# Performance work log

Measured on AMD Instinct MI355X. Metric: run time of the kernel, lower is better.

Reference implementation:

```python
import jax, jax.numpy as jnp
import numpy as np

EPS = 1e-5
NEG_SLOPE = 0.2


def knn(x, k):
    # x: (B, C, N). pairwise_distance = -||xi - xj||^2, topk -> nearest neighbors.
    xt = jnp.swapaxes(x, 1, 2)                       # (B, N, C)
    inner = -2.0 * jnp.matmul(xt, x)                 # (B, N, N)
    xx = jnp.sum(x * x, axis=1, keepdims=True)       # (B, 1, N)
    pd = -xx - inner - jnp.swapaxes(xx, 1, 2)        # (B, N, N)
    return jax.lax.top_k(pd, k)[1]                   # (B, N, k) int32


def get_graph_feature(x, k):
    # x: (B, C, N) -> (B, N, k, 2C) edge features [neighbor - center, center]
    idx = knn(x, k)
    xt = jnp.swapaxes(x, 1, 2)                       # (B, N, C)
    nb = jax.vmap(lambda f, i: f[i])(xt, idx)        # (B, N, k, C) gather
    center = xt[:, :, None, :]                       # (B, N, 1, C)
    return jnp.concatenate(
        [nb - center, jnp.broadcast_to(center, nb.shape)], axis=-1)


def edge_conv(x, w, k):
    # conv_2d with kernel 1: 1x1 conv (no bias) + InstanceNorm2d + LeakyReLU, then max over k
    feat = get_graph_feature(x, k)                   # (B, N, k, 2C)
    y = jnp.einsum('bnkc,oc->bonk', feat, w)         # (B, O, N, k)
    mean = jnp.mean(y, axis=(2, 3), keepdims=True)
    var = jnp.var(y, axis=(2, 3), keepdims=True)
    y = (y - mean) * jax.lax.rsqrt(var + EPS)        # InstanceNorm2d (no affine)
    y = jnp.where(y >= 0, y, NEG_SLOPE * y)
    return jnp.max(y, axis=-1)                       # (B, O, N)


def setup_inputs() -> dict:
    key = jax.random.key(0)
    ks = jax.random.split(key, 8)
    B, N = 16, 2048
    s = 0.05
    return {
        'x': jax.random.normal(ks[0], (B, 3, N), dtype=jnp.float32),
        'w1': jax.random.normal(ks[1], (64, 6), dtype=jnp.float32) * s,
        'w2': jax.random.normal(ks[2], (64, 128), dtype=jnp.float32) * s,
        'w3': jax.random.normal(ks[3], (128, 128), dtype=jnp.float32) * s,
        'w4': jax.random.normal(ks[4], (256, 256), dtype=jnp.float32) * s,
        'w5': jax.random.normal(ks[5], (512, 512), dtype=jnp.float32) * s,
        'bn5_gamma': jnp.ones((512,), dtype=jnp.float32),
        'bn5_beta': jnp.zeros((512,), dtype=jnp.float32),
    }


def reference(x, w1, w2, w3, w4, w5, bn5_gamma, bn5_beta):
    k = 20
    x1 = edge_conv(x, w1, k)                         # (B, 64, N)
    x2 = edge_conv(x1, w2, k)                        # (B, 64, N)
    x3 = edge_conv(x2, w3, k)                        # (B, 128, N)
    x4 = edge_conv(x3, w4, k)                        # (B, 256, N)
    x_cat = jnp.concatenate([x1, x2, x3, x4], axis=1)  # (B, 512, N)
    y = jnp.einsum('bcn,oc->bon', x_cat, w5)         # conv5, (B, 512, N)
    # BatchNorm1d (training-mode batch stats) over (B, N)
    mean = jnp.mean(y, axis=(0, 2), keepdims=True)
    var = jnp.var(y, axis=(0, 2), keepdims=True)
    y = (y - mean) * jax.lax.rsqrt(var + EPS)
    y = y * bn5_gamma[None, :, None] + bn5_beta[None, :, None]
    y = jnp.where(y >= 0, y, NEG_SLOPE * y)
    feat = jnp.concatenate([jnp.max(y, axis=2), jnp.mean(y, axis=2)], axis=1)  # (B, 1024)
    return feat
```

## Files before the change

### kernel.cpp

```cpp
#include <hip/hip_runtime.h>

#define NN 2048
#define NB 16
#define KK 20
#define EPSF 1e-5f

typedef unsigned long long ull;
typedef _Float16 v8h __attribute__((ext_vector_type(8)));
typedef float v4f __attribute__((ext_vector_type(4)));

__device__ __forceinline__ float shflx_f(float v, int m) { return __shfl_xor(v, m, 64); }
__device__ __forceinline__ ull shflx_u64(ull v, int m) {
  int lo = __shfl_xor((int)(unsigned)v, m, 64);
  int hi = __shfl_xor((int)(unsigned)(v >> 32), m, 64);
  return (((ull)(unsigned)hi) << 32) | (unsigned)lo;
}
__device__ __forceinline__ ull packkey(float s, int n) {
  unsigned u = __float_as_uint(s);
  u = (u & 0x80000000u) ? ~u : (u | 0x80000000u);
  return (((ull)u) << 32) | (unsigned)(2047 - n);
}

__global__ __launch_bounds__(256) void prep_kernel(const float* __restrict__ x,
    _Float16* __restrict__ xh, _Float16* __restrict__ xl, float* __restrict__ xx,
    int C, int KB, long bstride)
{
  const int b = blockIdx.y;
  const int n = blockIdx.x * 256 + threadIdx.x;
  const float* xb = x + (size_t)b * bstride;
  const int Cp = KB * 32;
  _Float16* ph = xh + ((size_t)b * NN + n) * Cp;
  _Float16* pl = xl + ((size_t)b * NN + n) * Cp;
  float s = 0.f;
  for (int kb = 0; kb < KB; kb++) {
    for (int g = 0; g < 4; g++) {
      v8h hv, lv;
#pragma unroll
      for (int j = 0; j < 8; j++) {
        int c = kb * 32 + g * 8 + j;
        float v = (c < C) ? xb[(size_t)c * NN + n] : 0.f;
        _Float16 h = (_Float16)v;
        hv[j] = h;
        lv[j] = (_Float16)(v - (float)h);
        s = fmaf(v, v, s);
      }
      *(v8h*)(ph + kb * 32 + g * 8) = hv;
      *(v8h*)(pl + kb * 32 + g * 8) = lv;
    }
  }
  xx[b * NN + n] = s;
}

template<int KB>
__device__ __forceinline__ void tile_scores(const v8h (&Bh)[KB], const v8h (&Bl)[KB],
    const v8h (&Ah)[4][KB], const v8h (&Al)[4][KB], float xv, v4f (&out)[4])
{
#pragma unroll
  for (int a = 0; a < 4; a++) {
    v4f a0 = {0.f, 0.f, 0.f, 0.f};
    v4f a1 = {0.f, 0.f, 0.f, 0.f};
#pragma unroll
    for (int kb = 0; kb < KB; kb++) {
      v4f& acc = (kb & 1) ? a1 : a0;
      acc = __builtin_amdgcn_mfma_f32_16x16x32_f16(Ah[a][kb], Bh[kb], acc, 0, 0, 0);
      acc = __builtin_amdgcn_mfma_f32_16x16x32_f16(Ah[a][kb], Bl[kb], acc, 0, 0, 0);
      acc = __builtin_amdgcn_mfma_f32_16x16x32_f16(Al[a][kb], Bh[kb], acc, 0, 0, 0);
    }
    v4f s = a0 + a1;
#pragma unroll
    for (int j = 0; j < 4; j++) out[a][j] = s[j] - 0.5f * xv;
  }
}

template<int KB>
__global__ __launch_bounds__(256, 1) void knn2(
    const _Float16* __restrict__ xh, const _Float16* __restrict__ xl,
    const float* __restrict__ xxg, ull* __restrict__ slistG, int* __restrict__ cntG)
{
  __shared__ float gmL[256][33];
  __shared__ float tauL[256];
  __shared__ int scnt[256];

  const int t = threadIdx.x;
  const int lane = t & 63;
  const int wave = t >> 6;
  const int col = lane & 15;
  const int quad = lane >> 4;
  const int quad8 = quad * 8;
  const int b = blockIdx.x >> 1;
  const int chunk = blockIdx.x & 1;
  const int qg = blockIdx.y;
  const int Cp = KB * 32;
  const int cb = chunk * 1024;
  const _Float16* xhb = xh + (size_t)b * NN * Cp;
  const _Float16* xlb = xl + (size_t)b * NN * Cp;
  const float* xxb = xxg + b * NN;

  v8h Ah[4][KB], Al[4][KB];
  const int qw = qg * 256 + wave * 64;
#pragma unroll
  for (int a = 0; a < 4; a++) {
    const _Float16* pa = xhb + (size_t)(qw + a * 16 + col) * Cp + quad8;
    const _Float16* pb = xlb + (size_t)(qw + a * 16 + col) * Cp + quad8;
#pragma unroll
    for (int kb = 0; kb < KB; kb++) {
      Ah[a][kb] = *(const v8h*)(pa + kb * 32);
      Al[a][kb] = *(const v8h*)(pb + kb * 32);
    }
  }

  v8h Bh[2][KB], Bl[2][KB];
  float xvb[2];
  auto loadB = [&](int slot, int tt) {
    int t2 = tt < 63 ? tt : 63;
    int n = cb + t2 * 16 + col;
    const _Float16* pb = xhb + (size_t)n * Cp + quad8;
    const _Float16* pl = xlb + (size_t)n * Cp + quad8;
#pragma unroll
    for (int kb = 0; kb < KB; kb++) {
      Bh[slot][kb] = *(const v8h*)(pb + kb * 32);
      Bl[slot][kb] = *(const v8h*)(pl + kb * 32);
    }
    xvb[slot] = xxb[n];
  };

  float gm[4][8];
#pragma unroll
  for (int a = 0; a < 4; a++)
#pragma unroll
    for (int j = 0; j < 8; j++) gm[a][j] = -3.4e38f;

  loadB(0, 0);
  for (int tt = 0; tt < 64; tt += 2) {
    loadB(1, tt + 1);
    {
      v4f out[4];
      tile_scores<KB>(Bh[0], Bl[0], Ah, Al, xvb[0], out);
#pragma unroll
      for (int a = 0; a < 4; a++)
#pragma unroll
        for (int j = 0; j < 4; j++) gm[a][j * 2] = fmaxf(gm[a][j * 2], out[a][j]);
    }
    loadB(0, tt + 2);
    {
      v4f out[4];
      tile_scores<KB>(Bh[1], Bl[1], Ah, Al, xvb[1], out);
#pragma unroll
      for (int a = 0; a < 4; a++)
#pragma unroll
        for (int j = 0; j < 4; j++) gm[a][j * 2 + 1] = fmaxf(gm[a][j * 2 + 1], out[a][j]);
    }
  }

#pragma unroll
  for (int a = 0; a < 4; a++)
#pragma unroll
    for (int j = 0; j < 4; j++) {
      int qi = wave * 64 + a * 16 + quad * 4 + j;
      gmL[qi][col * 2 + 0] = gm[a][j * 2 + 0];
      gmL[qi][col * 2 + 1] = gm[a][j * 2 + 1];
    }
  scnt[t] = 0;
  asm volatile("s_waitcnt lgkmcnt(0)" ::: "memory");

  for (int r = 0; r < 32; r++) {
    const int q = wave * 64 + r * 2 + (lane >> 5);
    const int idx = lane & 31;
    float v = gmL[q][idx];
#pragma unroll
    for (int kk = 2; kk <= 32; kk <<= 1) {
#pragma unroll
      for (int m = kk >> 1; m >= 1; m >>= 1) {
        float o = shflx_f(v, m);
        bool keepmax = ((idx & kk) == 0) == ((idx & m) == 0);
        v = keepmax ? fmaxf(v, o) : fminf(v, o);
      }
    }
    if (idx == 19) tauL[q] = v;
  }
  asm volatile("s_waitcnt lgkmcnt(0)" ::: "memory");

  float tq[4][4];
#pragma unroll
  for (int a = 0; a < 4; a++)
#pragma unroll
    for (int j = 0; j < 4; j++) tq[a][j] = tauL[wave * 64 + a * 16 + quad * 4 + j];

  ull* slB = slistG + (((size_t)b * NN + qg * 256) * 2 + chunk) * 64;
  loadB(0, 0);
  for (int tt = 0; tt < 64; tt += 2) {
    loadB(1, tt + 1);
    for (int s = 0; s < 2; s++) {
      v4f out[4];
      tile_scores<KB>(s ? Bh[1] : Bh[0], s ? Bl[1] : Bl[0], Ah, Al, xvb[s], out);
      int n = cb + (tt + s) * 16 + col;
#pragma unroll
      for (int a = 0; a < 4; a++)
#pragma unroll
        for (int j = 0; j < 4; j++) {
          float sc = out[a][j];
          if (sc >= tq[a][j]) {
            int qi = wave * 64 + a * 16 + quad * 4 + j;
            int pos = atomicAdd(&scnt[qi], 1);
            if (pos < 64) slB[(size_t)qi * 128 + pos] = packkey(sc, n);
          }
        }
      if (s == 0) loadB(0, tt + 2);
    }
  }
  asm volatile("s_waitcnt lgkmcnt(0)" ::: "memory");
  cntG[((size_t)b * NN + qg * 256 + t) * 2 + chunk] = scnt[t];
}

__global__ __launch_bounds__(256) void knn_merge(const ull* __restrict__ slistG,
    const int* __restrict__ cntG, const _Float16* __restrict__ xh,
    const _Float16* __restrict__ xl, const float* __restrict__ xxg,
    int* __restrict__ idxout, int Cp, int C)
{
  const int lane = threadIdx.x & 63, wave = threadIdx.x >> 6;
  const int b = blockIdx.y;
  const int q = blockIdx.x * 4 + wave;
  const int c0 = cntG[((size_t)b * NN + q) * 2 + 0];
  const int c1 = cntG[((size_t)b * NN + q) * 2 + 1];
  int* op = idxout + ((size_t)b * NN + q) * KK;

  if (c0 <= 64 && c1 <= 64) {
    const ull* s0 = slistG + ((size_t)b * NN + q) * 128;
    const int total = c0 + c1;
    ull e0 = 0, e1 = 0;
    int p0 = lane, p1 = lane + 64;
    if (p0 < total) e0 = (p0 < c0) ? s0[p0] : s0[64 + p0 - c0];
    if (p1 < total) e1 = (p1 < c0) ? s0[p1] : s0[64 + p1 - c0];
    for (int s = 0; s < KK; s++) {
      ull m = e0 > e1 ? e0 : e1;
      ull g = m;
#pragma unroll
      for (int d = 1; d < 64; d <<= 1) { ull o = shflx_u64(g, d); g = o > g ? o : g; }
      if (lane == 0) op[s] = 2047 - (int)(g & 0xFFFFFFFFu);
      if (e0 == g) e0 = 0; else if (e1 == g) e1 = 0;
    }
  } else {
    const _Float16* qh = xh + ((size_t)b * NN + q) * Cp;
    const _Float16* ql = xl + ((size_t)b * NN + q) * Cp;
    const float* xxb = xxg + b * NN;
    float sc[32];
#pragma unroll
    for (int i = 0; i < 32; i++) sc[i] = -0.5f * xxb[lane + 64 * i];
    for (int c = 0; c < C; c++) {
      float qv = (float)qh[c] + (float)ql[c];
      for (int i = 0; i < 32; i++) {
        int n = lane + 64 * i;
        float bv = (float)xh[((size_t)b * NN + n) * Cp + c] + (float)xl[((size_t)b * NN + n) * Cp + c];
        sc[i] = fmaf(qv, bv, sc[i]);
      }
    }
    for (int s = 0; s < KK; s++) {
      ull m = 0; int mi = -1;
      for (int i = 0; i < 32; i++) {
        ull k = packkey(sc[i], lane + 64 * i);
        if (k > m) { m = k; mi = i; }
      }
      ull g = m;
#pragma unroll
      for (int d = 1; d < 64; d <<= 1) { ull o = shflx_u64(g, d); g = o > g ? o : g; }
      if (lane == 0) op[s] = 2047 - (int)(g & 0xFFFFFFFFu);
      if (m == g && mi >= 0) sc[mi] = -3.4e38f;
    }
  }
}

__global__ __launch_bounds__(256) void wcvt_uv(const float* __restrict__ w,
    _Float16* __restrict__ wuh, _Float16* __restrict__ wul,
    _Float16* __restrict__ wvh, _Float16* __restrict__ wvl, int C, int Cp, int O)
{
  int idx = blockIdx.x * 256 + threadIdx.x;
  if (idx >= O * Cp) return;
  int o = idx / Cp, c = idx - o * Cp;
  float a = 0.f, bv = 0.f;
  if (c < C) { a = w[o * 2 * C + c]; bv = w[o * 2 * C + C + c]; }
  float v = bv - a;
  _Float16 ah = (_Float16)a; wuh[idx] = ah; wul[idx] = (_Float16)(a - (float)ah);
  _Float16 vh = (_Float16)v; wvh[idx] = vh; wvl[idx] = (_Float16)(v - (float)vh);
}

__global__ __launch_bounds__(256) void w5cvt(const float* __restrict__ w5,
    _Float16* __restrict__ w5h, _Float16* __restrict__ w5l)
{
  int idx = blockIdx.x * 256 + threadIdx.x;
  float v = w5[idx];
  _Float16 h = (_Float16)v;
  w5h[idx] = h;
  w5l[idx] = (_Float16)(v - (float)h);
}

__global__ __launch_bounds__(256) void y5cvt_kernel(const float* __restrict__ xcat,
    _Float16* __restrict__ xh, _Float16* __restrict__ xl)
{
  const int b = blockIdx.y;
  const int n = blockIdx.x * 256 + threadIdx.x;
  for (int kc = blockIdx.z * 4; kc < blockIdx.z * 4 + 4; kc++) {
    v8h h[4], l[4];
#pragma unroll
    for (int g = 0; g < 4; g++)
#pragma unroll
      for (int j = 0; j < 8; j++) {
        float v = xcat[((size_t)b * 512 + kc * 32 + g * 8 + j) * NN + n];
        _Float16 hh = (_Float16)v;
        h[g][j] = hh;
        l[g][j] = (_Float16)(v - (float)hh);
      }
    size_t base = (((size_t)b * 16 + kc) * NN + n) * 32;
#pragma unroll
    for (int g = 0; g < 4; g++) {
      *(v8h*)(xh + base + g * 8) = h[g];
      *(v8h*)(xl + base + g * 8) = l[g];
    }
  }
}

__global__ __launch_bounds__(256) void y5_mfma(const _Float16* __restrict__ w5h,
    const _Float16* __restrict__ w5l, const _Float16* __restrict__ xh,
    const _Float16* __restrict__ xl, float* __restrict__ y5)
{
  const int lane = threadIdx.x & 63, wave = threadIdx.x >> 6;
  const int col = lane & 15, quad = lane >> 4, quad8 = quad * 8;
  const int b = blockIdx.z;
  const int o0 = blockIdx.x * 256 + wave * 64;
  const int nb0 = blockIdx.y * 128;
  v4f acc[4][8];
#pragma unroll
  for (int a = 0; a < 4; a++)
#pragma unroll
    for (int t = 0; t < 8; t++) acc[a][t] = {0.f, 0.f, 0.f, 0.f};

  for (int kc = 0; kc < 16; kc++) {
    v8h Ah[4], Al[4];
#pragma unroll
    for (int a = 0; a < 4; a++) {
      size_t off = (size_t)(o0 + a * 16 + col) * 512 + kc * 32 + quad8;
      Ah[a] = *(const v8h*)(w5h + off);
      Al[a] = *(const v8h*)(w5l + off);
    }
#pragma unroll
    for (int t = 0; t < 8; t++) {
      int n = nb0 + t * 16 + col;
      size_t boff = (((size_t)b * 16 + kc) * NN + n) * 32 + quad8;
      v8h Bh = *(const v8h*)(xh + boff);
      v8h Bl = *(const v8h*)(xl + boff);
#pragma unroll
      for (int a = 0; a < 4; a++) {
        acc[a][t] = __builtin_amdgcn_mfma_f32_16x16x32_f16(Ah[a], Bh, acc[a][t], 0, 0, 0);
        acc[a][t] = __builtin_amdgcn_mfma_f32_16x16x32_f16(Ah[a], Bl, acc[a][t], 0, 0, 0);
        acc[a][t] = __builtin_amdgcn_mfma_f32_16x16x32_f16(Al[a], Bh, acc[a][t], 0, 0, 0);
      }
    }
  }
#pragma unroll
  for (int a = 0; a < 4; a++)
#pragma unroll
    for (int t = 0; t < 8; t++)
#pragma unroll
      for (int j = 0; j < 4; j++)
        y5[((size_t)b * 512 + o0 + a * 16 + quad * 4 + j) * NN + nb0 + t * 16 + col] = acc[a][t][j];
}

__global__ __launch_bounds__(256) void uv_mfma(const _Float16* __restrict__ wuh,
    const _Float16* __restrict__ wul, const _Float16* __restrict__ wvh,
    const _Float16* __restrict__ wvl, const _Float16* __restrict__ xh,
    const _Float16* __restrict__ xl, float* __restrict__ Uc, float* __restrict__ Vc,
    int Cp, int Och)
{
  const int lane = threadIdx.x & 63, wave = threadIdx.x >> 6;
  const int col = lane & 15, quad = lane >> 4, quad8 = quad * 8;
  const int b = blockIdx.z;
  const int o0 = blockIdx.x * 32;
  const int nb0 = blockIdx.y * 256 + wave * 64;
  v4f aU[2][4], aV[2][4];
#pragma unroll
  for (int a = 0; a < 2; a++)
#pragma unroll
    for (int t = 0; t < 4; t++) { aU[a][t] = {0.f,0.f,0.f,0.f}; aV[a][t] = {0.f,0.f,0.f,0.f}; }

  const int KBr = Cp >> 5;
  for (int kb = 0; kb < KBr; kb++) {
    v8h Uh[2], Ul[2], Vh[2], Vl[2];
#pragma unroll
    for (int a = 0; a < 2; a++) {
      size_t off = (size_t)(o0 + a * 16 + col) * Cp + kb * 32 + quad8;
      Uh[a] = *(const v8h*)(wuh + off);
      Ul[a] = *(const v8h*)(wul + off);
      Vh[a] = *(const v8h*)(wvh + off);
      Vl[a] = *(const v8h*)(wvl + off);
    }
#pragma unroll
    for (int t = 0; t < 4; t++) {
      int n = nb0 + t * 16 + col;
      size_t boff = ((size_t)b * NN + n) * Cp + kb * 32 + quad8;
      v8h Bh = *(const v8h*)(xh + boff);
      v8h Bl = *(const v8h*)(xl + boff);
#pragma unroll
      for (int a = 0; a < 2; a++) {
        aU[a][t] = __builtin_amdgcn_mfma_f32_16x16x32_f16(Uh[a], Bh, aU[a][t], 0, 0, 0);
        aU[a][t] = __builtin_amdgcn_mfma_f32_16x16x32_f16(Uh[a], Bl, aU[a][t], 0, 0, 0);
        aU[a][t] = __builtin_amdgcn_mfma_f32_16x16x32_f16(Ul[a], Bh, aU[a][t], 0, 0, 0);
        aV[a][t] = __builtin_amdgcn_mfma_f32_16x16x32_f16(Vh[a], Bh, aV[a][t], 0, 0, 0);
        aV[a][t] = __builtin_amdgcn_mfma_f32_16x16x32_f16(Vh[a], Bl, aV[a][t], 0, 0, 0);
        aV[a][t] = __builtin_amdgcn_mfma_f32_16x16x32_f16(Vl[a], Bh, aV[a][t], 0, 0, 0);
      }
    }
  }
#pragma unroll
  for (int a = 0; a < 2; a++)
#pragma unroll
    for (int t = 0; t < 4; t++)
#pragma unroll
      for (int j = 0; j < 4; j++) {
        size_t base = ((size_t)b * Och + o0 + a * 16 + quad * 4 + j) * NN + nb0 + t * 16 + col;
        Uc[base] = aU[a][t][j];
        Vc[base] = aV[a][t][j];
      }
}

__global__ __launch_bounds__(256) void edge5(const float* __restrict__ Uc,
    const float* __restrict__ Vc, const int* __restrict__ idx,
    float* __restrict__ xo, int Och)
{
  __shared__ float Ur[2 * 2052];
  __shared__ float red[4][4];
  __shared__ float smv[4];
  const int b = blockIdx.y, o0 = blockIdx.x * 2;
  const int t = threadIdx.x, lane = t & 63, wave = t >> 6;
  for (int r = 0; r < 2; r++)
    for (int i = t; i < NN; i += 256)
      Ur[r * 2052 + i] = Uc[((size_t)b * Och + o0 + r) * NN + i];
  __syncthreads();
  const float* Vp = Vc + ((size_t)b * Och + o0) * NN;
  const int* ib = idx + (size_t)b * NN * KK;
  float s0 = 0, s1 = 0, c0 = 0, c1 = 0;
  for (int n = t; n < NN; n += 256) {
    float v0 = Vp[n], v1 = Vp[NN + n];
    const int* ip = ib + (size_t)n * KK;
#pragma unroll
    for (int j = 0; j < KK; j++) {
      int m = ip[j];
      float y0 = Ur[m] + v0, y1 = Ur[2052 + m] + v1;
      s0 += y0; c0 = fmaf(y0, y0, c0);
      s1 += y1; c1 = fmaf(y1, y1, c1);
    }
  }
  float st[4] = { s0, s1, c0, c1 };
#pragma unroll
  for (int k = 0; k < 4; k++) {
    float a = st[k];
#pragma unroll
    for (int d = 1; d < 64; d <<= 1) a += shflx_f(a, d);
    if (lane == 0) red[k][wave] = a;
  }
  __syncthreads();
  if (t < 2) {
    float a = red[t][0] + red[t][1] + red[t][2] + red[t][3];
    float c = red[2 + t][0] + red[2 + t][1] + red[2 + t][2] + red[2 + t][3];
    const float inv = 1.f / (float)(NN * KK);
    float mu = a * inv;
    float var = fmaxf(c * inv - mu * mu, 0.f);
    smv[t] = mu;
    smv[2 + t] = rsqrtf(var + EPSF);
  }
  __syncthreads();
  const float mu0 = smv[0], mu1 = smv[1], i0 = smv[2], i1 = smv[3];
  for (int n = t; n < NN; n += 256) {
    float v0 = Vp[n], v1 = Vp[NN + n];
    const int* ip = ib + (size_t)n * KK;
    float m0 = -3.4e38f, m1 = m0;
#pragma unroll
    for (int j = 0; j < KK; j++) {
      int m = ip[j];
      m0 = fmaxf(m0, Ur[m] + v0);
      m1 = fmaxf(m1, Ur[2052 + m] + v1);
    }
    float z;
    z = (m0 - mu0) * i0; xo[((size_t)b * 512 + o0 + 0) * NN + n] = z >= 0.f ? z : 0.2f * z;
    z = (m1 - mu1) * i1; xo[((size_t)b * 512 + o0 + 1) * NN + n] = z >= 0.f ? z : 0.2f * z;
  }
}

__global__ __launch_bounds__(256) void bn5stat_kernel(const float* __restrict__ y5,
    float* __restrict__ bn5) {
  __shared__ float rs[4], rq[4];
  const int o = blockIdx.x, t = threadIdx.x, lane = t & 63, wave = t >> 6;
  float s = 0.f, q = 0.f;
  for (int b = 0; b < NB; b++) {
    const float* p = y5 + ((size_t)b * 512 + o) * NN;
    for (int n = t; n < NN; n += 256) { float v = p[n]; s += v; q = fmaf(v, v, q); }
  }
#pragma unroll
  for (int d = 1; d < 64; d <<= 1) { s += shflx_f(s, d); q += shflx_f(q, d); }
  if (lane == 0) { rs[wave] = s; rq[wave] = q; }
  __syncthreads();
  if (t == 0) {
    float S = rs[0] + rs[1] + rs[2] + rs[3];
    float Q = rq[0] + rq[1] + rq[2] + rq[3];
    const float inv = 1.f / (float)(NB * NN);
    float mu = S * inv;
    float var = fmaxf(Q * inv - mu * mu, 0.f);
    bn5[o] = mu;
    bn5[512 + o] = rsqrtf(var + EPSF);
  }
}

__global__ __launch_bounds__(256) void final_kernel(const float* __restrict__ y5,
    const float* __restrict__ bn5, const float* __restrict__ gamma,
    const float* __restrict__ beta, float* __restrict__ out)
{
  __shared__ float rm[4], rs[4];
  const int o = blockIdx.x, b = blockIdx.y, t = threadIdx.x, lane = t & 63, wave = t >> 6;
  const float mu = bn5[o], iv = bn5[512 + o], g = gamma[o], be = beta[o];
  const float* p = y5 + ((size_t)b * 512 + o) * NN;
  float mx = -3.4e38f, sm = 0.f;
  for (int n = t; n < NN; n += 256) {
    float z = (p[n] - mu) * iv;
    z = z * g + be;
    z = (z >= 0.f) ? z : 0.2f * z;
    mx = fmaxf(mx, z);
    sm += z;
  }
#pragma unroll
  for (int d = 1; d < 64; d <<= 1) { mx = fmaxf(mx, shflx_f(mx, d)); sm += shflx_f(sm, d); }
  if (lane == 0) { rm[wave] = mx; rs[wave] = sm; }
  __syncthreads();
  if (t == 0) {
    float M = fmaxf(fmaxf(rm[0], rm[1]), fmaxf(rm[2], rm[3]));
    float S = rs[0] + rs[1] + rs[2] + rs[3];
    out[(size_t)b * 1024 + o] = M;
    out[(size_t)b * 1024 + 512 + o] = S * (1.f / NN);
  }
}

extern "C" void kernel_launch(void* const* d_in, const int* in_sizes, int n_in,
                              void* d_out, int out_size, void* d_ws, size_t ws_size,
                              hipStream_t stream)
{
  (void)in_sizes; (void)n_in; (void)out_size; (void)ws_size;
  const float* x  = (const float*)d_in[0];
  const float* w1 = (const float*)d_in[1];
  const float* w2 = (const float*)d_in[2];
  const float* w3 = (const float*)d_in[3];
  const float* w4 = (const float*)d_in[4];
  const float* w5 = (const float*)d_in[5];
  const float* g5 = (const float*)d_in[6];
  const float* b5 = (const float*)d_in[7];
  float* out = (float*)d_out;

  float* ws   = (float*)d_ws;
  float* xcat = ws;
  float* Ub   = xcat + 16777216;
  float* Vb   = Ub + 8388608;
  int*   idxb = (int*)(Vb + 8388608);
  float* xxb  = (float*)(idxb + 655360);
  float* bn5  = xxb + 32768;

  _Float16* xth = (_Float16*)Vb;
  _Float16* xtl = xth + 4194304;
  int* cntb = (int*)(Vb + 4194304);
  _Float16* wuh = (_Float16*)(Vb + 4259840);
  _Float16* wul = wuh + 32768;
  _Float16* wvh = wul + 32768;
  _Float16* wvl = wvh + 32768;

  ull* slist = (ull*)Ub;
  float* Uc = Ub;
  float* Vc = Ub + 4194304;

  _Float16* w5h = (_Float16*)idxb;
  _Float16* w5l = w5h + 262144;
  _Float16* xcfh = (_Float16*)Ub;
  _Float16* xcfl = (_Float16*)Vb;
  float* y5 = xcat;

  struct Lyr { const float* xin; long bstride; int C, KB, O, coff; const float* w; };
  const Lyr L[4] = {
    { x,              3L * NN,   3,   1, 64,  0,   w1 },
    { xcat,           512L * NN, 64,  2, 64,  64,  w2 },
    { xcat + 64 * NN, 512L * NN, 64,  2, 128, 128, w3 },
    { xcat + 128 * NN,512L * NN, 128, 4, 256, 256, w4 },
  };

  for (int l = 0; l < 4; l++) {
    const int Cp = L[l].KB * 32, O = L[l].O, C = L[l].C;
    prep_kernel<<<dim3(NN / 256, NB), 256, 0, stream>>>(L[l].xin, xth, xtl, xxb,
                                                        C, L[l].KB, L[l].bstride);
    switch (L[l].KB) {
      case 1: knn2<1><<<dim3(NB * 2, NN / 256), 256, 0, stream>>>(xth, xtl, xxb, slist, cntb); break;
      case 2: knn2<2><<<dim3(NB * 2, NN / 256), 256, 0, stream>>>(xth, xtl, xxb, slist, cntb); break;
      default: knn2<4><<<dim3(NB * 2, NN / 256), 256, 0, stream>>>(xth, xtl, xxb, slist, cntb); break;
    }
    knn_merge<<<dim3(NN / 4, NB), 256, 0, stream>>>(slist, cntb, xth, xtl, xxb, idxb,
                                                    Cp, C);
    wcvt_uv<<<(O * Cp + 255) / 256, 256, 0, stream>>>(L[l].w, wuh, wul, wvh, wvl,
                                                      C, Cp, O);
    for (int c0 = 0; c0 < O; c0 += 128) {
      const int Och = (O - c0) < 128 ? (O - c0) : 128;
      uv_mfma<<<dim3(Och / 32, NN / 256, NB), 256, 0, stream>>>(
          wuh + (size_t)c0 * Cp, wul + (size_t)c0 * Cp,
          wvh + (size_t)c0 * Cp, wvl + (size_t)c0 * Cp,
          xth, xtl, Uc, Vc, Cp, Och);
      edge5<<<dim3(Och / 2, NB), 256, 0, stream>>>(Uc, Vc, idxb,
          xcat + (size_t)(L[l].coff + c0) * NN, Och);
    }
  }
  w5cvt<<<1024, 256, 0, stream>>>(w5, w5h, w5l);
  y5cvt_kernel<<<dim3(NN / 256, NB, 4), 256, 0, stream>>>(xcat, xcfh, xcfl);
  y5_mfma<<<dim3(2, NN / 128, NB), 256, 0, stream>>>(w5h, w5l, xcfh, xcfl, y5);
  bn5stat_kernel<<<512, 256, 0, stream>>>(y5, bn5);
  final_kernel<<<dim3(512, NB), 256, 0, stream>>>(y5, bn5, g5, b5, out);
}
```

Baseline: 1.636 ms.

## Split KNN candidate columns into four chunks with 512-thread blocks

Restructures the KNN scoring kernel so each block covers 512 queries with 8 waves, and the 2048 candidate columns are split into four 512-wide chunks instead of two 1024-wide ones. The grid changes from 32x8 blocks of 256 threads to 64x4 blocks of 512 threads, launched with an occupancy hint of two blocks per CU. Each chunk keeps its own per-query threshold and candidate list. The extra two chunk lists are stored in spare space in the xcat buffer for columns that later layers have not yet written, and the merge kernel now combines four lists instead of two. Per-chunk thresholds over fewer columns are looser, so more candidates pass and overflow into the slow fallback path is more likely, and the larger shared gmL array may limit occupancy.

```diff
diff --git a/kernel.cpp b/kernel.cpp
--- a/kernel.cpp
+++ b/kernel.cpp
@@ -73,13 +73,14 @@
 }
 
 template<int KB>
-__global__ __launch_bounds__(256, 1) void knn2(
+__global__ __launch_bounds__(512, 2) void knn4(
     const _Float16* __restrict__ xh, const _Float16* __restrict__ xl,
-    const float* __restrict__ xxg, ull* __restrict__ slistG, int* __restrict__ cntG)
-{
-  __shared__ float gmL[256][33];
-  __shared__ float tauL[256];
-  __shared__ int scnt[256];
+    const float* __restrict__ xxg, ull* __restrict__ slist1,
+    ull* __restrict__ sl2, int coff, int* __restrict__ cntG)
+{
+  __shared__ float gmL[512][33];
+  __shared__ float tauL[512];
+  __shared__ int scnt[512];
 
   const int t = threadIdx.x;
   const int lane = t & 63;
@@ -87,17 +88,17 @@
   const int col = lane & 15;
   const int quad = lane >> 4;
   const int quad8 = quad * 8;
-  const int b = blockIdx.x >> 1;
-  const int chunk = blockIdx.x & 1;
+  const int b = blockIdx.x >> 2;
+  const int chunk = blockIdx.x & 3;
   const int qg = blockIdx.y;
   const int Cp = KB * 32;
-  const int cb = chunk * 1024;
+  const int cb = chunk * 512;
   const _Float16* xhb = xh + (size_t)b * NN * Cp;
   const _Float16* xlb = xl + (size_t)b * NN * Cp;
   const float* xxb = xxg + b * NN;
 
   v8h Ah[4][KB], Al[4][KB];
-  const int qw = qg * 256 + wave * 64;
+  const int qw = qg * 512 + wave * 64;
 #pragma unroll
   for (int a = 0; a < 4; a++) {
     const _Float16* pa = xhb + (size_t)(qw + a * 16 + col) * Cp + quad8;
@@ -112,7 +113,7 @@
   v8h Bh[2][KB], Bl[2][KB];
   float xvb[2];
   auto loadB = [&](int slot, int tt) {
-    int t2 = tt < 63 ? tt : 63;
+    int t2 = tt < 31 ? tt : 31;
     int n = cb + t2 * 16 + col;
     const _Float16* pb = xhb + (size_t)n * Cp + quad8;
     const _Float16* pl = xlb + (size_t)n * Cp + quad8;
@@ -131,7 +132,7 @@
     for (int j = 0; j < 8; j++) gm[a][j] = -3.4e38f;
 
   loadB(0, 0);
-  for (int tt = 0; tt < 64; tt += 2) {
+  for (int tt = 0; tt < 32; tt += 2) {
     loadB(1, tt + 1);
     {
       v4f out[4];
@@ -186,9 +187,11 @@
 #pragma unroll
     for (int j = 0; j < 4; j++) tq[a][j] = tauL[wave * 64 + a * 16 + quad * 4 + j];
 
-  ull* slB = slistG + (((size_t)b * NN + qg * 256) * 2 + chunk) * 64;
+  ull* slq0 = (chunk < 2)
+      ? slist1 + ((size_t)b * NN + qg * 512) * 128 + chunk * 64
+      : sl2 + ((size_t)b * 512 + coff) * 1024 + (size_t)(qg * 512) * 128 + (chunk - 2) * 64;
   loadB(0, 0);
-  for (int tt = 0; tt < 64; tt += 2) {
+  for (int tt = 0; tt < 32; tt += 2) {
     loadB(1, tt + 1);
     for (int s = 0; s < 2; s++) {
       v4f out[4];
@@ -202,42 +205,58 @@
           if (sc >= tq[a][j]) {
             int qi = wave * 64 + a * 16 + quad * 4 + j;
             int pos = atomicAdd(&scnt[qi], 1);
-            if (pos < 64) slB[(size_t)qi * 128 + pos] = packkey(sc, n);
+            if (pos < 64) slq0[(size_t)qi * 128 + pos] = packkey(sc, n);
           }
         }
       if (s == 0) loadB(0, tt + 2);
     }
   }
   asm volatile("s_waitcnt lgkmcnt(0)" ::: "memory");
-  cntG[((size_t)b * NN + qg * 256 + t) * 2 + chunk] = scnt[t];
-}
-
-__global__ __launch_bounds__(256) void knn_merge(const ull* __restrict__ slistG,
-    const int* __restrict__ cntG, const _Float16* __restrict__ xh,
-    const _Float16* __restrict__ xl, const float* __restrict__ xxg,
-    int* __restrict__ idxout, int Cp, int C)
+  cntG[((size_t)b * NN + qg * 512 + t) * 4 + chunk] = scnt[t];
+}
+
+__global__ __launch_bounds__(256) void knn_merge4(const ull* __restrict__ slist1,
+    const ull* __restrict__ sl2, int coff, const int* __restrict__ cntG,
+    const _Float16* __restrict__ xh, const _Float16* __restrict__ xl,
+    const float* __restrict__ xxg, int* __restrict__ idxout, int Cp, int C)
 {
   const int lane = threadIdx.x & 63, wave = threadIdx.x >> 6;
   const int b = blockIdx.y;
   const int q = blockIdx.x * 4 + wave;
-  const int c0 = cntG[((size_t)b * NN + q) * 2 + 0];
-  const int c1 = cntG[((size_t)b * NN + q) * 2 + 1];
-  int* op = idxout + ((size_t)b * NN + q) * KK;
-
-  if (c0 <= 64 && c1 <= 64) {
-    const ull* s0 = slistG + ((size_t)b * NN + q) * 128;
-    const int total = c0 + c1;
-    ull e0 = 0, e1 = 0;
-    int p0 = lane, p1 = lane + 64;
-    if (p0 < total) e0 = (p0 < c0) ? s0[p0] : s0[64 + p0 - c0];
-    if (p1 < total) e1 = (p1 < c0) ? s0[p1] : s0[64 + p1 - c0];
+  const size_t qb = (size_t)b * NN + q;
+  const int c0 = cntG[qb * 4 + 0], c1 = cntG[qb * 4 + 1];
+  const int c2 = cntG[qb * 4 + 2], c3 = cntG[qb * 4 + 3];
+  int* op = idxout + qb * KK;
+
+  if (c0 <= 64 && c1 <= 64 && c2 <= 64 && c3 <= 64) {
+    const ull* seg01 = slist1 + qb * 128;
+    const ull* seg23 = sl2 + ((size_t)b * 512 + coff) * 1024 + (size_t)q * 128;
+    const int O1 = c0, O2 = c0 + c1, O3 = c0 + c1 + c2, tot = O3 + c3;
+    ull e[4];
+#pragma unroll
+    for (int i = 0; i < 4; i++) {
+      int p = lane + i * 64;
+      ull v = 0;
+      if (p < tot) {
+        if (p < O1)      v = seg01[p];
+        else if (p < O2) v = seg01[64 + p - O1];
+        else if (p < O3) v = seg23[p - O2];
+        else             v = seg23[64 + p - O3];
+      }
+      e[i] = v;
+    }
     for (int s = 0; s < KK; s++) {
-      ull m = e0 > e1 ? e0 : e1;
+      ull m = e[0] > e[1] ? e[0] : e[1];
+      ull m2 = e[2] > e[3] ? e[2] : e[3];
+      m = m > m2 ? m : m2;
       ull g = m;
 #pragma unroll
       for (int d = 1; d < 64; d <<= 1) { ull o = shflx_u64(g, d); g = o > g ? o : g; }
       if (lane == 0) op[s] = 2047 - (int)(g & 0xFFFFFFFFu);
-      if (e0 == g) e0 = 0; else if (e1 == g) e1 = 0;
+      if (e[0] == g) e[0] = 0;
+      else if (e[1] == g) e[1] = 0;
+      else if (e[2] == g) e[2] = 0;
+      else if (e[3] == g) e[3] = 0;
     }
   } else {
     const _Float16* qh = xh + ((size_t)b * NN + q) * Cp;
@@ -562,12 +581,13 @@
   _Float16* xth = (_Float16*)Vb;
   _Float16* xtl = xth + 4194304;
   int* cntb = (int*)(Vb + 4194304);
-  _Float16* wuh = (_Float16*)(Vb + 4259840);
+  _Float16* wuh = (_Float16*)(Vb + 4325376);
   _Float16* wul = wuh + 32768;
   _Float16* wvh = wul + 32768;
   _Float16* wvl = wvh + 32768;
 
   ull* slist = (ull*)Ub;
+  ull* sl2   = (ull*)xcat;
   float* Uc = Ub;
   float* Vc = Ub + 4194304;
 
@@ -586,16 +606,16 @@
   };
 
   for (int l = 0; l < 4; l++) {
-    const int Cp = L[l].KB * 32, O = L[l].O, C = L[l].C;
+    const int Cp = L[l].KB * 32, O = L[l].O, C = L[l].C, coff = L[l].coff;
     prep_kernel<<<dim3(NN / 256, NB), 256, 0, stream>>>(L[l].xin, xth, xtl, xxb,
                                                         C, L[l].KB, L[l].bstride);
     switch (L[l].KB) {
-      case 1: knn2<1><<<dim3(NB * 2, NN / 256), 256, 0, stream>>>(xth, xtl, xxb, slist, cntb); break;
-      case 2: knn2<2><<<dim3(NB * 2, NN / 256), 256, 0, stream>>>(xth, xtl, xxb, slist, cntb); break;
-      default: knn2<4><<<dim3(NB * 2, NN / 256), 256, 0, stream>>>(xth, xtl, xxb, slist, cntb); break;
-    }
-    knn_merge<<<dim3(NN / 4, NB), 256, 0, stream>>>(slist, cntb, xth, xtl, xxb, idxb,
-                                                    Cp, C);
+      case 1: knn4<1><<<dim3(NB * 4, 4), 512, 0, stream>>>(xth, xtl, xxb, slist, sl2, coff, cntb); break;
+      case 2: knn4<2><<<dim3(NB * 4, 4), 512, 0, stream>>>(xth, xtl, xxb, slist, sl2, coff, cntb); break;
+      default: knn4<4><<<dim3(NB * 4, 4), 512, 0, stream>>>(xth, xtl, xxb, slist, sl2, coff, cntb); break;
+    }
+    knn_merge4<<<dim3(NN / 4, NB), 256, 0, stream>>>(slist, sl2, coff, cntb,
+                                                     xth, xtl, xxb, idxb, Cp, C);
     wcvt_uv<<<(O * Cp + 255) / 256, 256, 0, stream>>>(L[l].w, wuh, wul, wvh, wvl,
                                                       C, Cp, O);
     for (int c0 = 0; c0 < O; c0 += 128) {
```

Measured after the change: 1.900 ms. 16.1% more time.

## Stage kNN candidate tiles through double-buffered shared memory in knn kernel

Applied to the files above, without the earlier changes.

In the kNN score kernel, each wave used to load the 16-point candidate B tile (fp16 hi/lo parts) straight from global memory into registers, so the four waves each fetched the same data. Now the block loads each tile once, using a register prefetch for the next tile, writes it into padded double-buffered LDS, and every wave reads its MFMA operands from LDS. This cuts redundant global traffic and register pressure. In exchange it adds a __syncthreads per tile and halves the per-iteration unroll, which could expose latency.

```diff
diff --git a/kernel.cpp b/kernel.cpp
--- a/kernel.cpp
+++ b/kernel.cpp
@@ -73,13 +73,17 @@
 }
 
 template<int KB>
-__global__ __launch_bounds__(256, 1) void knn2(
+__global__ __launch_bounds__(256, 1) void knn5(
     const _Float16* __restrict__ xh, const _Float16* __restrict__ xl,
     const float* __restrict__ xxg, ull* __restrict__ slistG, int* __restrict__ cntG)
 {
+  constexpr int Cp = KB * 32;
+  constexpr int RS = Cp + 8;
   __shared__ float gmL[256][33];
   __shared__ float tauL[256];
   __shared__ int scnt[256];
+  __shared__ _Float16 sBh[2][16 * RS];
+  __shared__ _Float16 sBl[2][16 * RS];
 
   const int t = threadIdx.x;
   const int lane = t & 63;
@@ -90,7 +94,6 @@
   const int b = blockIdx.x >> 1;
   const int chunk = blockIdx.x & 1;
   const int qg = blockIdx.y;
-  const int Cp = KB * 32;
   const int cb = chunk * 1024;
   const _Float16* xhb = xh + (size_t)b * NN * Cp;
   const _Float16* xlb = xl + (size_t)b * NN * Cp;
@@ -109,20 +112,24 @@
     }
   }
 
-  v8h Bh[2][KB], Bl[2][KB];
-  float xvb[2];
-  auto loadB = [&](int slot, int tt) {
+  constexpr int NL = (16 * Cp) / 8;
+  const int ci = t / (Cp / 8);
+  const int c8 = (t % (Cp / 8)) * 8;
+  v8h rH, rL;
+  auto stageG = [&](int tt) {
     int t2 = tt < 63 ? tt : 63;
-    int n = cb + t2 * 16 + col;
-    const _Float16* pb = xhb + (size_t)n * Cp + quad8;
-    const _Float16* pl = xlb + (size_t)n * Cp + quad8;
-#pragma unroll
-    for (int kb = 0; kb < KB; kb++) {
-      Bh[slot][kb] = *(const v8h*)(pb + kb * 32);
-      Bl[slot][kb] = *(const v8h*)(pl + kb * 32);
-    }
-    xvb[slot] = xxb[n];
+    if (t < NL) {
+      size_t off = (size_t)(cb + t2 * 16 + ci) * Cp + c8;
+      rH = *(const v8h*)(xhb + off);
+      rL = *(const v8h*)(xlb + off);
+    }
   };
+  auto stageW = [&](int buf) {
+    if (t < NL) {
+      *(v8h*)&sBh[buf][ci * RS + c8] = rH;
+      *(v8h*)&sBl[buf][ci * RS + c8] = rL;
+    }
+  };
 
   float gm[4][8];
 #pragma unroll
@@ -130,26 +137,28 @@
 #pragma unroll
     for (int j = 0; j < 8; j++) gm[a][j] = -3.4e38f;
 
-  loadB(0, 0);
-  for (int tt = 0; tt < 64; tt += 2) {
-    loadB(1, tt + 1);
+  stageG(0); stageW(0); __syncthreads();
+  for (int tt = 0; tt < 64; tt++) {
+    stageG(tt + 1);
     {
+      const int buf = tt & 1;
+      float xv = xxb[cb + tt * 16 + col];
+      v8h Bh[KB], Bl[KB];
+#pragma unroll
+      for (int kb = 0; kb < KB; kb++) {
+        Bh[kb] = *(const v8h*)&sBh[buf][col * RS + kb * 32 + quad8];
+        Bl[kb] = *(const v8h*)&sBl[buf][col * RS + kb * 32 + quad8];
+      }
       v4f out[4];
-      tile_scores<KB>(Bh[0], Bl[0], Ah, Al, xvb[0], out);
+      tile_scores<KB>(Bh, Bl, Ah, Al, xv, out);
+      const int par = tt & 1;
 #pragma unroll
       for (int a = 0; a < 4; a++)
 #pragma unroll
-        for (int j = 0; j < 4; j++) gm[a][j * 2] = fmaxf(gm[a][j * 2], out[a][j]);
-    }
-    loadB(0, tt + 2);
-    {
-      v4f out[4];
-      tile_scores<KB>(Bh[1], Bl[1], Ah, Al, xvb[1], out);
-#pragma unroll
-      for (int a = 0; a < 4; a++)
-#pragma unroll
-        for (int j = 0; j < 4; j++) gm[a][j * 2 + 1] = fmaxf(gm[a][j * 2 + 1], out[a][j]);
-    }
+        for (int j = 0; j < 4; j++) gm[a][j * 2 + par] = fmaxf(gm[a][j * 2 + par], out[a][j]);
+    }
+    stageW((tt + 1) & 1);
+    __syncthreads();
   }
 
 #pragma unroll
@@ -187,13 +196,21 @@
     for (int j = 0; j < 4; j++) tq[a][j] = tauL[wave * 64 + a * 16 + quad * 4 + j];
 
   ull* slB = slistG + (((size_t)b * NN + qg * 256) * 2 + chunk) * 64;
-  loadB(0, 0);
-  for (int tt = 0; tt < 64; tt += 2) {
-    loadB(1, tt + 1);
-    for (int s = 0; s < 2; s++) {
+  stageG(0); stageW(0); __syncthreads();
+  for (int tt = 0; tt < 64; tt++) {
+    stageG(tt + 1);
+    {
+      const int buf = tt & 1;
+      float xv = xxb[cb + tt * 16 + col];
+      v8h Bh[KB], Bl[KB];
+#pragma unroll
+      for (int kb = 0; kb < KB; kb++) {
+        Bh[kb] = *(const v8h*)&sBh[buf][col * RS + kb * 32 + quad8];
+        Bl[kb] = *(const v8h*)&sBl[buf][col * RS + kb * 32 + quad8];
+      }
       v4f out[4];
-      tile_scores<KB>(s ? Bh[1] : Bh[0], s ? Bl[1] : Bl[0], Ah, Al, xvb[s], out);
-      int n = cb + (tt + s) * 16 + col;
+      tile_scores<KB>(Bh, Bl, Ah, Al, xv, out);
+      int n = cb + tt * 16 + col;
 #pragma unroll
       for (int a = 0; a < 4; a++)
 #pragma unroll
@@ -205,8 +222,9 @@
             if (pos < 64) slB[(size_t)qi * 128 + pos] = packkey(sc, n);
           }
         }
-      if (s == 0) loadB(0, tt + 2);
-    }
+    }
+    stageW((tt + 1) & 1);
+    __syncthreads();
   }
   asm volatile("s_waitcnt lgkmcnt(0)" ::: "memory");
   cntG[((size_t)b * NN + qg * 256 + t) * 2 + chunk] = scnt[t];
@@ -590,9 +608,9 @@
     prep_kernel<<<dim3(NN / 256, NB), 256, 0, stream>>>(L[l].xin, xth, xtl, xxb,
                                                         C, L[l].KB, L[l].bstride);
     switch (L[l].KB) {
-      case 1: knn2<1><<<dim3(NB * 2, NN / 256), 256, 0, stream>>>(xth, xtl, xxb, slist, cntb); break;
-      case 2: knn2<2><<<dim3(NB * 2, NN / 256), 256, 0, stream>>>(xth, xtl, xxb, slist, cntb); break;
-      default: knn2<4><<<dim3(NB * 2, NN / 256), 256, 0, stream>>>(xth, xtl, xxb, slist, cntb); break;
+      case 1: knn5<1><<<dim3(NB * 2, NN / 256), 256, 0, stream>>>(xth, xtl, xxb, slist, cntb); break;
+      case 2: knn5<2><<<dim3(NB * 2, NN / 256), 256, 0, stream>>>(xth, xtl, xxb, slist, cntb); break;
+      default: knn5<4><<<dim3(NB * 2, NN / 256), 256, 0, stream>>>(xth, xtl, xxb, slist, cntb); break;
     }
     knn_merge<<<dim3(NN / 4, NB), 256, 0, stream>>>(slist, cntb, xth, xtl, xxb, idxb,
                                                     Cp, C);
```

New measurement: 1.737 ms. 6.2% more time.

## Decompose edge-conv instance-norm stats into U/V sums with neighbor-count histogram

Applied to the files above, without the earlier changes.

Builds a per-batch histogram of how often each point appears as a neighbor, fused into the weight-conversion kernel. The edge kernel then gets the variance from per-point sums of U, V, V·G and count-weighted U², so the gather loop only sums and maxes U. It also keeps the per-point max in registers, so the second gather pass over the neighbor indices goes away. The costs are an extra kernel phase with shared-memory atomics, more registers, and a change in float accumulation order for the variance.

```diff
diff --git a/kernel.cpp b/kernel.cpp
--- a/kernel.cpp
+++ b/kernel.cpp
@@ -269,18 +269,33 @@
   }
 }
 
-__global__ __launch_bounds__(256) void wcvt_uv(const float* __restrict__ w,
+__global__ __launch_bounds__(256) void setup_kernel(const int* __restrict__ idx,
+    int* __restrict__ cnt, const float* __restrict__ w,
     _Float16* __restrict__ wuh, _Float16* __restrict__ wul,
-    _Float16* __restrict__ wvh, _Float16* __restrict__ wvl, int C, int Cp, int O)
-{
-  int idx = blockIdx.x * 256 + threadIdx.x;
-  if (idx >= O * Cp) return;
-  int o = idx / Cp, c = idx - o * Cp;
-  float a = 0.f, bv = 0.f;
-  if (c < C) { a = w[o * 2 * C + c]; bv = w[o * 2 * C + C + c]; }
-  float v = bv - a;
-  _Float16 ah = (_Float16)a; wuh[idx] = ah; wul[idx] = (_Float16)(a - (float)ah);
-  _Float16 vh = (_Float16)v; wvh[idx] = vh; wvl[idx] = (_Float16)(v - (float)vh);
+    _Float16* __restrict__ wvh, _Float16* __restrict__ wvl,
+    int C, int Cp, int O)
+{
+  __shared__ int h[2048];
+  const int blk = blockIdx.x, t = threadIdx.x;
+  if (blk < NB) {
+    const int b = blk;
+    for (int i = t; i < 2048; i += 256) h[i] = 0;
+    __syncthreads();
+    const int* ib = idx + (size_t)b * NN * KK;
+    for (int i = t; i < NN * KK; i += 256) atomicAdd(&h[ib[i]], 1);
+    __syncthreads();
+    for (int i = t; i < 2048; i += 256) cnt[b * 2048 + i] = h[i];
+  } else {
+    int e = (blk - NB) * 256 + t;
+    if (e < O * Cp) {
+      int o = e / Cp, c = e - o * Cp;
+      float a = 0.f, bv = 0.f;
+      if (c < C) { a = w[o * 2 * C + c]; bv = w[o * 2 * C + C + c]; }
+      float v = bv - a;
+      _Float16 ah = (_Float16)a; wuh[e] = ah; wul[e] = (_Float16)(a - (float)ah);
+      _Float16 vh = (_Float16)v; wvh[e] = vh; wvl[e] = (_Float16)(v - (float)vh);
+    }
+  }
 }
 
 __global__ __launch_bounds__(256) void w5cvt(const float* __restrict__ w5,
@@ -421,12 +436,12 @@
       }
 }
 
-__global__ __launch_bounds__(256) void edge5(const float* __restrict__ Uc,
+__global__ __launch_bounds__(256) void edge6(const float* __restrict__ Uc,
     const float* __restrict__ Vc, const int* __restrict__ idx,
-    float* __restrict__ xo, int Och)
+    const int* __restrict__ cnt, float* __restrict__ xo, int Och)
 {
   __shared__ float Ur[2 * 2052];
-  __shared__ float red[4][4];
+  __shared__ float red[10][4];
   __shared__ float smv[4];
   const int b = blockIdx.y, o0 = blockIdx.x * 2;
   const int t = threadIdx.x, lane = t & 63, wave = t >> 6;
@@ -436,21 +451,38 @@
   __syncthreads();
   const float* Vp = Vc + ((size_t)b * Och + o0) * NN;
   const int* ib = idx + (size_t)b * NN * KK;
-  float s0 = 0, s1 = 0, c0 = 0, c1 = 0;
-  for (int n = t; n < NN; n += 256) {
-    float v0 = Vp[n], v1 = Vp[NN + n];
+  const int* cb = cnt + b * NN;
+
+  float sG0 = 0, sG1 = 0, sVG0 = 0, sVG1 = 0, sV0 = 0, sV1 = 0;
+  float sV20 = 0, sV21 = 0, sU20 = 0, sU21 = 0;
+  float Mr[2][8];
+#pragma unroll
+  for (int ni = 0; ni < 8; ni++) {
+    const int n = t + ni * 256;
     const int* ip = ib + (size_t)n * KK;
+    float G0 = 0, G1 = 0;
+    float M0 = -3.4e38f, M1 = M0;
 #pragma unroll
     for (int j = 0; j < KK; j++) {
       int m = ip[j];
-      float y0 = Ur[m] + v0, y1 = Ur[2052 + m] + v1;
-      s0 += y0; c0 = fmaf(y0, y0, c0);
-      s1 += y1; c1 = fmaf(y1, y1, c1);
-    }
-  }
-  float st[4] = { s0, s1, c0, c1 };
-#pragma unroll
-  for (int k = 0; k < 4; k++) {
+      float u0 = Ur[m], u1 = Ur[2052 + m];
+      G0 += u0; M0 = fmaxf(M0, u0);
+      G1 += u1; M1 = fmaxf(M1, u1);
+    }
+    float v0 = Vp[n], v1 = Vp[NN + n];
+    sG0 += G0; sVG0 = fmaf(v0, G0, sVG0); sV0 += v0; sV20 = fmaf(v0, v0, sV20);
+    sG1 += G1; sVG1 = fmaf(v1, G1, sVG1); sV1 += v1; sV21 = fmaf(v1, v1, sV21);
+    Mr[0][ni] = M0; Mr[1][ni] = M1;
+  }
+  for (int i = t; i < NN; i += 256) {
+    float c = (float)cb[i];
+    float u0 = Ur[i], u1 = Ur[2052 + i];
+    sU20 = fmaf(c * u0, u0, sU20);
+    sU21 = fmaf(c * u1, u1, sU21);
+  }
+  float st[10] = { sG0, sG1, sVG0, sVG1, sV0, sV1, sV20, sV21, sU20, sU21 };
+#pragma unroll
+  for (int k = 0; k < 10; k++) {
     float a = st[k];
 #pragma unroll
     for (int d = 1; d < 64; d <<= 1) a += shflx_f(a, d);
@@ -458,29 +490,29 @@
   }
   __syncthreads();
   if (t < 2) {
-    float a = red[t][0] + red[t][1] + red[t][2] + red[t][3];
-    float c = red[2 + t][0] + red[2 + t][1] + red[2 + t][2] + red[2 + t][3];
+    float g  = red[t][0] + red[t][1] + red[t][2] + red[t][3];
+    float vg = red[2 + t][0] + red[2 + t][1] + red[2 + t][2] + red[2 + t][3];
+    float v  = red[4 + t][0] + red[4 + t][1] + red[4 + t][2] + red[4 + t][3];
+    float v2 = red[6 + t][0] + red[6 + t][1] + red[6 + t][2] + red[6 + t][3];
+    float u2 = red[8 + t][0] + red[8 + t][1] + red[8 + t][2] + red[8 + t][3];
+    float sumY  = g + (float)KK * v;
+    float sumY2 = u2 + 2.f * vg + (float)KK * v2;
     const float inv = 1.f / (float)(NN * KK);
-    float mu = a * inv;
-    float var = fmaxf(c * inv - mu * mu, 0.f);
+    float mu = sumY * inv;
+    float var = fmaxf(sumY2 * inv - mu * mu, 0.f);
     smv[t] = mu;
     smv[2 + t] = rsqrtf(var + EPSF);
   }
   __syncthreads();
   const float mu0 = smv[0], mu1 = smv[1], i0 = smv[2], i1 = smv[3];
-  for (int n = t; n < NN; n += 256) {
-    float v0 = Vp[n], v1 = Vp[NN + n];
-    const int* ip = ib + (size_t)n * KK;
-    float m0 = -3.4e38f, m1 = m0;
-#pragma unroll
-    for (int j = 0; j < KK; j++) {
-      int m = ip[j];
-      m0 = fmaxf(m0, Ur[m] + v0);
-      m1 = fmaxf(m1, Ur[2052 + m] + v1);
-    }
+#pragma unroll
+  for (int ni = 0; ni < 8; ni++) {
+    const int n = t + ni * 256;
     float z;
-    z = (m0 - mu0) * i0; xo[((size_t)b * 512 + o0 + 0) * NN + n] = z >= 0.f ? z : 0.2f * z;
-    z = (m1 - mu1) * i1; xo[((size_t)b * 512 + o0 + 1) * NN + n] = z >= 0.f ? z : 0.2f * z;
+    z = (Mr[0][ni] + Vp[n] - mu0) * i0;
+    xo[((size_t)b * 512 + o0 + 0) * NN + n] = z >= 0.f ? z : 0.2f * z;
+    z = (Mr[1][ni] + Vp[NN + n] - mu1) * i1;
+    xo[((size_t)b * 512 + o0 + 1) * NN + n] = z >= 0.f ? z : 0.2f * z;
   }
 }
 
@@ -566,6 +598,7 @@
   _Float16* wul = wuh + 32768;
   _Float16* wvh = wul + 32768;
   _Float16* wvl = wvh + 32768;
+  int* cnth = (int*)(Vb + 4325376);
 
   ull* slist = (ull*)Ub;
   float* Uc = Ub;
@@ -596,15 +629,16 @@
     }
     knn_merge<<<dim3(NN / 4, NB), 256, 0, stream>>>(slist, cntb, xth, xtl, xxb, idxb,
                                                     Cp, C);
-    wcvt_uv<<<(O * Cp + 255) / 256, 256, 0, stream>>>(L[l].w, wuh, wul, wvh, wvl,
-                                                      C, Cp, O);
+    const int wblocks = (O * Cp + 255) / 256;
+    setup_kernel<<<NB + wblocks, 256, 0, stream>>>(idxb, cnth, L[l].w,
+        wuh, wul, wvh, wvl, C, Cp, O);
     for (int c0 = 0; c0 < O; c0 += 128) {
       const int Och = (O - c0) < 128 ? (O - c0) : 128;
       uv_mfma<<<dim3(Och / 32, NN / 256, NB), 256, 0, stream>>>(
           wuh + (size_t)c0 * Cp, wul + (size_t)c0 * Cp,
           wvh + (size_t)c0 * Cp, wvl + (size_t)c0 * Cp,
           xth, xtl, Uc, Vc, Cp, Och);
-      edge5<<<dim3(Och / 2, NB), 256, 0, stream>>>(Uc, Vc, idxb,
+      edge6<<<dim3(Och / 2, NB), 256, 0, stream>>>(Uc, Vc, idxb, cnth,
           xcat + (size_t)(L[l].coff + c0) * NN, Och);
     }
   }
```

New measurement: 1.887 ms. +15.3%, slower.
